# Performance work log

Hardware: AMD Instinct MI355X
Metric: run time of the kernel (lower is better)

## Reference

```python
import jax, jax.numpy as jnp
import numpy as np

BINS = 10
LOSS_WEIGHT = 1.0


def setup_inputs() -> dict:
    key = jax.random.key(0)
    k1, k2 = jax.random.split(key)
    N, C = 32768, 1024
    pred = jax.random.normal(k1, (N, C), dtype=jnp.float32)
    target = jax.random.randint(k2, (N,), 0, C, dtype=jnp.int32)
    return {"pred": pred, "target": target}


def reference(pred, target):
    N, C = pred.shape
    # one-hot target (torch scatter_ of 1 at label index)
    t = jax.nn.one_hot(target, C, dtype=pred.dtype)  # [N, C]
    # gradient norm g = |sigmoid(pred).detach() - target|, in [0, 1]
    g = jnp.abs(jax.nn.sigmoid(jax.lax.stop_gradient(pred)) - t)
    # all samples valid (label_weight=None -> ones); tot = max(sum(valid), 1)
    tot = jnp.asarray(N * C, dtype=pred.dtype)
    # edges = arange(bins+1)/bins with edges[-1] += 1e-6: bin = floor(g*bins),
    # g == 1.0 falls in last bin -> clip to bins-1
    bin_idx = jnp.clip((g * BINS).astype(jnp.int32), 0, BINS - 1)  # [N, C]
    counts = jnp.bincount(bin_idx.ravel(), length=BINS).astype(pred.dtype)  # [BINS]
    nonempty = counts > 0
    n = jnp.maximum(jnp.sum(nonempty).astype(pred.dtype), 1.0)
    # per-bin weight tot/num_in_bin for nonempty bins, then divide by n
    w_bin = jnp.where(nonempty, tot / jnp.maximum(counts, 1.0), 0.0) / n
    weights = w_bin[bin_idx]  # gather back to [N, C]
    # stable BCE-with-logits, weighted, reduction='sum'
    bce = jnp.maximum(pred, 0.0) - pred * t + jnp.log1p(jnp.exp(-jnp.abs(pred)))
    loss = jnp.sum(weights * bce) / tot
    return loss * LOSS_WEIGHT
```

## Files before the change

### kernel.cpp

```cpp
#include <hip/hip_runtime.h>
#include <math.h>


#define PASS1_BLOCK 256

__device__ __forceinline__ void wave_red(float& v) {
#pragma unroll
    for (int off = 32; off > 0; off >>= 1) v += __shfl_down(v, off, 64);
}
__device__ __forceinline__ void wave_red(unsigned& v) {
#pragma unroll
    for (int off = 32; off > 0; off >>= 1) v += __shfl_down(v, off, 64);
}

__device__ __forceinline__ void update_elem(float p, bool isT,
                                            float (&S)[10], unsigned (&Cc)[9]) {
    const float T[9] = {-2.1972246f, -1.3862944f, -0.84729786f, -0.40546511f,
                        0.0f, 0.40546511f, 0.84729786f, 1.3862944f, 2.1972246f};
    float s = isT ? -p : p;
    float a = fabsf(s);
    float en = __expf(-a);
    float bce = fmaxf(s, 0.0f) + __logf(1.0f + en);
    S[0] += bce;
#pragma unroll
    for (int q = 0; q < 9; ++q) {
        bool b = (s >= T[q]);
        S[q + 1] += b ? bce : 0.0f;
        Cc[q] += b ? 1u : 0u;
    }
}

__global__ __launch_bounds__(PASS1_BLOCK) void ghmc_pass1(
    const float* __restrict__ pred, const int* __restrict__ target,
    float* __restrict__ blk_S, unsigned* __restrict__ blk_C,
    unsigned total4, unsigned totalNC, int C, int shift) {
    float S[10];
    unsigned Cc[9];
#pragma unroll
    for (int i = 0; i < 10; ++i) S[i] = 0.0f;
#pragma unroll
    for (int i = 0; i < 9; ++i) Cc[i] = 0u;

    unsigned tid = blockIdx.x * blockDim.x + threadIdx.x;
    unsigned stride = gridDim.x * blockDim.x;
    const float4* p4 = (const float4*)pred;
    unsigned cmask = (unsigned)C - 1u;

    for (unsigned v = tid; v < total4; v += stride) {
        unsigned e = v << 2;
        unsigned row, col;
        if (shift >= 0) {
            row = e >> shift;
            col = e & cmask;
        } else {
            row = e / (unsigned)C;
            col = e - row * (unsigned)C;
        }
        float4 p = p4[v];
        int tj = target[row];
        update_elem(p.x, tj == (int)(col + 0u), S, Cc);
        update_elem(p.y, tj == (int)(col + 1u), S, Cc);
        update_elem(p.z, tj == (int)(col + 2u), S, Cc);
        update_elem(p.w, tj == (int)(col + 3u), S, Cc);
    }

    if (tid == 0) {
        for (unsigned e = total4 << 2; e < totalNC; ++e) {
            unsigned row, col;
            if (shift >= 0) {
                row = e >> shift;
                col = e & cmask;
            } else {
                row = e / (unsigned)C;
                col = e - row * (unsigned)C;
            }
            update_elem(pred[e], target[row] == (int)col, S, Cc);
        }
    }

#pragma unroll
    for (int i = 0; i < 10; ++i) wave_red(S[i]);
#pragma unroll
    for (int i = 0; i < 9; ++i) wave_red(Cc[i]);

    __shared__ float sS[PASS1_BLOCK / 64][10];
    __shared__ unsigned sC[PASS1_BLOCK / 64][9];
    int wid = threadIdx.x >> 6;
    int lane = threadIdx.x & 63;
    if (lane == 0) {
        for (int i = 0; i < 10; ++i) sS[wid][i] = S[i];
        for (int i = 0; i < 9; ++i) sC[wid][i] = Cc[i];
    }
    __syncthreads();
    if (threadIdx.x == 0) {
        const int nw = PASS1_BLOCK / 64;
        for (int i = 0; i < 10; ++i) {
            float acc = 0.0f;
            for (int w = 0; w < nw; ++w) acc += sS[w][i];
            blk_S[blockIdx.x * 10 + i] = acc;
        }
        for (int i = 0; i < 9; ++i) {
            unsigned acc = 0u;
            for (int w = 0; w < nw; ++w) acc += sC[w][i];
            blk_C[blockIdx.x * 9 + i] = acc;
        }
    }
}

__global__ __launch_bounds__(256) void ghmc_pass2(
    const float* __restrict__ blk_S, const unsigned* __restrict__ blk_C,
    float* __restrict__ out, int nblocks, unsigned totalNC) {
    float S[10];
    unsigned Cc[9];
#pragma unroll
    for (int i = 0; i < 10; ++i) S[i] = 0.0f;
#pragma unroll
    for (int i = 0; i < 9; ++i) Cc[i] = 0u;

    for (int b = threadIdx.x; b < nblocks; b += blockDim.x) {
        for (int i = 0; i < 10; ++i) S[i] += blk_S[b * 10 + i];
        for (int i = 0; i < 9; ++i) Cc[i] += blk_C[b * 9 + i];
    }

#pragma unroll
    for (int i = 0; i < 10; ++i) wave_red(S[i]);
#pragma unroll
    for (int i = 0; i < 9; ++i) wave_red(Cc[i]);

    __shared__ float sS[4][10];
    __shared__ unsigned sC[4][9];
    int wid = threadIdx.x >> 6;
    int lane = threadIdx.x & 63;
    if (lane == 0) {
        for (int i = 0; i < 10; ++i) sS[wid][i] = S[i];
        for (int i = 0; i < 9; ++i) sC[wid][i] = Cc[i];
    }
    __syncthreads();
    if (threadIdx.x == 0) {
        float Sv[11];
        unsigned Cv[11];
        for (int i = 0; i < 10; ++i) {
            float a = 0.0f;
            for (int w = 0; w < 4; ++w) a += sS[w][i];
            Sv[i] = a;
        }
        Sv[10] = 0.0f;
        Cv[0] = totalNC;
        for (int i = 1; i < 10; ++i) {
            unsigned a = 0u;
            for (int w = 0; w < 4; ++w) a += sC[w][i - 1];
            Cv[i] = a;
        }
        Cv[10] = 0u;

        int nonempty = 0;
        for (int b = 0; b < 10; ++b)
            if (Cv[b] - Cv[b + 1] > 0u) nonempty++;
        float n = fmaxf((float)nonempty, 1.0f);

        float loss = 0.0f;
        for (int b = 0; b < 10; ++b) {
            unsigned cnt = Cv[b] - Cv[b + 1];
            if (cnt > 0u) {
                float bs = Sv[b] - Sv[b + 1];
                loss += bs / ((float)cnt * n);
            }
        }
        out[0] = loss;
    }
}

extern "C" void kernel_launch(void* const* d_in, const int* in_sizes, int n_in,
                              void* d_out, int out_size, void* d_ws, size_t ws_size,
                              hipStream_t stream) {
    const float* pred = (const float*)d_in[0];
    const int* target = (const int*)d_in[1];
    int NC = in_sizes[0];
    int N = in_sizes[1];
    int C = NC / N;
    unsigned total4 = (unsigned)(NC / 4);
    int shift = ((C & (C - 1)) == 0) ? (__builtin_ctz((unsigned)C) + 0) : -1;

    int blocks = 1024;
    size_t per_block = (10 + 9) * sizeof(float);
    if (ws_size < (size_t)blocks * per_block) {
        size_t maxb = ws_size / per_block;
        blocks = (int)(maxb > 0 ? maxb : 1);
    }

    float* blk_S = (float*)d_ws;
    unsigned* blk_C = (unsigned*)((char*)d_ws + (size_t)blocks * 10 * sizeof(float));

    ghmc_pass1<<<blocks, PASS1_BLOCK, 0, stream>>>(pred, target, blk_S, blk_C,
                                                   total4, (unsigned)NC, C, shift);
    ghmc_pass2<<<1, 256, 0, stream>>>(blk_S, blk_C, (float*)d_out, blocks,
                                      (unsigned)NC);
}
```

Measured before the change: 210.4 us.

## Treat all elements as non-target and apply a per-row target correction

The hot loop no longer computes row and column indices or loads the target per element. Every element is processed as if its one-hot label were 0. A separate per-row step then reads the target logit once and adds the difference between the target and non-target BCE and bin contributions. Bin sums and counts are packed into 2-wide float vectors so the compiler can emit packed FMAs. The change also uses nontemporal vector loads and a doubled grid. Counts become floats, which trades exactness at very large totals for cheaper packed arithmetic. The correction assumes the grid has at least as many threads as there are rows.

New measurement: 218.5 us. +3.9%, slower.

```diff
diff --git a/kernel.cpp b/kernel.cpp
--- a/kernel.cpp
+++ b/kernel.cpp
@@ -3,167 +3,157 @@
 
 
 #define PASS1_BLOCK 256
+#define PASS1_GRID 2048
+
+typedef float v2f __attribute__((ext_vector_type(2)));
+typedef float v4f __attribute__((ext_vector_type(4)));
 
 __device__ __forceinline__ void wave_red(float& v) {
 #pragma unroll
     for (int off = 32; off > 0; off >>= 1) v += __shfl_down(v, off, 64);
 }
-__device__ __forceinline__ void wave_red(unsigned& v) {
-#pragma unroll
-    for (int off = 32; off > 0; off >>= 1) v += __shfl_down(v, off, 64);
-}
 
-__device__ __forceinline__ void update_elem(float p, bool isT,
-                                            float (&S)[10], unsigned (&Cc)[9]) {
-    const float T[9] = {-2.1972246f, -1.3862944f, -0.84729786f, -0.40546511f,
-                        0.0f, 0.40546511f, 0.84729786f, 1.3862944f, 2.1972246f};
-    float s = isT ? -p : p;
-    float a = fabsf(s);
+__device__ __constant__ float kThresh[9] = {
+    -2.1972246f, -1.3862944f, -0.84729786f, -0.40546511f, 0.0f,
+    0.40546511f, 0.84729786f, 1.3862944f, 2.1972246f};
+
+__device__ __forceinline__ void upd(float p, float& S0, v2f (&A)[9]) {
+    float a = fabsf(p);
     float en = __expf(-a);
-    float bce = fmaxf(s, 0.0f) + __logf(1.0f + en);
-    S[0] += bce;
+    float l1p = __logf(1.0f + en);
+    float bce = fmaxf(p, 0.0f) + l1p;
+    S0 += bce;
+    v2f bv = {bce, 1.0f};
 #pragma unroll
     for (int q = 0; q < 9; ++q) {
-        bool b = (s >= T[q]);
-        S[q + 1] += b ? bce : 0.0f;
-        Cc[q] += b ? 1u : 0u;
+        float m = (p >= kThresh[q]) ? 1.0f : 0.0f;
+        v2f mv = {m, m};
+        A[q] += bv * mv;
     }
 }
 
-__global__ __launch_bounds__(PASS1_BLOCK) void ghmc_pass1(
+__device__ __forceinline__ void upd_corr(float p, float& S0, v2f (&A)[9]) {
+    float a = fabsf(p);
+    float en = __expf(-a);
+    float l1p = __logf(1.0f + en);
+    float bf = fmaxf(p, 0.0f) + l1p;
+    float bt = fmaxf(-p, 0.0f) + l1p;
+    S0 += bt - bf;
+#pragma unroll
+    for (int q = 0; q < 9; ++q) {
+        float mf = (p >= kThresh[q]) ? 1.0f : 0.0f;
+        float mt = (-p >= kThresh[q]) ? 1.0f : 0.0f;
+        v2f d = {mt * bt - mf * bf, mt - mf};
+        A[q] += d;
+    }
+}
+
+__global__ __launch_bounds__(PASS1_BLOCK, 8) void ghmc_pass1(
     const float* __restrict__ pred, const int* __restrict__ target,
-    float* __restrict__ blk_S, unsigned* __restrict__ blk_C,
-    unsigned total4, unsigned totalNC, int C, int shift) {
-    float S[10];
-    unsigned Cc[9];
+    float* __restrict__ blk, unsigned total4, unsigned totalNC, int N, int C) {
+    float S0 = 0.0f;
+    v2f A[9];
 #pragma unroll
-    for (int i = 0; i < 10; ++i) S[i] = 0.0f;
-#pragma unroll
-    for (int i = 0; i < 9; ++i) Cc[i] = 0u;
+    for (int i = 0; i < 9; ++i) A[i] = (v2f){0.0f, 0.0f};
 
     unsigned tid = blockIdx.x * blockDim.x + threadIdx.x;
     unsigned stride = gridDim.x * blockDim.x;
-    const float4* p4 = (const float4*)pred;
-    unsigned cmask = (unsigned)C - 1u;
+    const v4f* p4 = (const v4f*)pred;
 
     for (unsigned v = tid; v < total4; v += stride) {
-        unsigned e = v << 2;
-        unsigned row, col;
-        if (shift >= 0) {
-            row = e >> shift;
-            col = e & cmask;
-        } else {
-            row = e / (unsigned)C;
-            col = e - row * (unsigned)C;
-        }
-        float4 p = p4[v];
-        int tj = target[row];
-        update_elem(p.x, tj == (int)(col + 0u), S, Cc);
-        update_elem(p.y, tj == (int)(col + 1u), S, Cc);
-        update_elem(p.z, tj == (int)(col + 2u), S, Cc);
-        update_elem(p.w, tj == (int)(col + 3u), S, Cc);
+        v4f p = __builtin_nontemporal_load(p4 + v);
+        upd(p[0], S0, A);
+        upd(p[1], S0, A);
+        upd(p[2], S0, A);
+        upd(p[3], S0, A);
     }
 
     if (tid == 0) {
-        for (unsigned e = total4 << 2; e < totalNC; ++e) {
-            unsigned row, col;
-            if (shift >= 0) {
-                row = e >> shift;
-                col = e & cmask;
-            } else {
-                row = e / (unsigned)C;
-                col = e - row * (unsigned)C;
-            }
-            update_elem(pred[e], target[row] == (int)col, S, Cc);
-        }
+        for (unsigned e = total4 << 2; e < totalNC; ++e) upd(pred[e], S0, A);
     }
 
+    int row = (int)(blockIdx.x * blockDim.x + threadIdx.x);
+    if (row < N) {
+        int t = target[row];
+        float p = pred[(unsigned)row * (unsigned)C + (unsigned)t];
+        upd_corr(p, S0, A);
+    }
+
+    float vals[19];
+    vals[0] = S0;
 #pragma unroll
-    for (int i = 0; i < 10; ++i) wave_red(S[i]);
+    for (int i = 0; i < 9; ++i) {
+        vals[1 + i] = A[i].x;
+        vals[10 + i] = A[i].y;
+    }
 #pragma unroll
-    for (int i = 0; i < 9; ++i) wave_red(Cc[i]);
+    for (int i = 0; i < 19; ++i) wave_red(vals[i]);
 
-    __shared__ float sS[PASS1_BLOCK / 64][10];
-    __shared__ unsigned sC[PASS1_BLOCK / 64][9];
+    __shared__ float sP[PASS1_BLOCK / 64][19];
     int wid = threadIdx.x >> 6;
     int lane = threadIdx.x & 63;
     if (lane == 0) {
-        for (int i = 0; i < 10; ++i) sS[wid][i] = S[i];
-        for (int i = 0; i < 9; ++i) sC[wid][i] = Cc[i];
+#pragma unroll
+        for (int i = 0; i < 19; ++i) sP[wid][i] = vals[i];
     }
     __syncthreads();
     if (threadIdx.x == 0) {
         const int nw = PASS1_BLOCK / 64;
-        for (int i = 0; i < 10; ++i) {
+#pragma unroll
+        for (int i = 0; i < 19; ++i) {
             float acc = 0.0f;
-            for (int w = 0; w < nw; ++w) acc += sS[w][i];
-            blk_S[blockIdx.x * 10 + i] = acc;
-        }
-        for (int i = 0; i < 9; ++i) {
-            unsigned acc = 0u;
-            for (int w = 0; w < nw; ++w) acc += sC[w][i];
-            blk_C[blockIdx.x * 9 + i] = acc;
+            for (int w = 0; w < nw; ++w) acc += sP[w][i];
+            blk[(unsigned)blockIdx.x * 19u + (unsigned)i] = acc;
         }
     }
 }
 
 __global__ __launch_bounds__(256) void ghmc_pass2(
-    const float* __restrict__ blk_S, const unsigned* __restrict__ blk_C,
-    float* __restrict__ out, int nblocks, unsigned totalNC) {
-    float S[10];
-    unsigned Cc[9];
+    const float* __restrict__ blk, float* __restrict__ out, int nblocks,
+    float totalNC) {
+    float P[19];
 #pragma unroll
-    for (int i = 0; i < 10; ++i) S[i] = 0.0f;
-#pragma unroll
-    for (int i = 0; i < 9; ++i) Cc[i] = 0u;
+    for (int i = 0; i < 19; ++i) P[i] = 0.0f;
 
     for (int b = threadIdx.x; b < nblocks; b += blockDim.x) {
-        for (int i = 0; i < 10; ++i) S[i] += blk_S[b * 10 + i];
-        for (int i = 0; i < 9; ++i) Cc[i] += blk_C[b * 9 + i];
+#pragma unroll
+        for (int i = 0; i < 19; ++i) P[i] += blk[(unsigned)b * 19u + (unsigned)i];
     }
+#pragma unroll
+    for (int i = 0; i < 19; ++i) wave_red(P[i]);
 
-#pragma unroll
-    for (int i = 0; i < 10; ++i) wave_red(S[i]);
-#pragma unroll
-    for (int i = 0; i < 9; ++i) wave_red(Cc[i]);
-
-    __shared__ float sS[4][10];
-    __shared__ unsigned sC[4][9];
+    __shared__ float sP[4][19];
     int wid = threadIdx.x >> 6;
     int lane = threadIdx.x & 63;
     if (lane == 0) {
-        for (int i = 0; i < 10; ++i) sS[wid][i] = S[i];
-        for (int i = 0; i < 9; ++i) sC[wid][i] = Cc[i];
+#pragma unroll
+        for (int i = 0; i < 19; ++i) sP[wid][i] = P[i];
     }
     __syncthreads();
     if (threadIdx.x == 0) {
-        float Sv[11];
-        unsigned Cv[11];
-        for (int i = 0; i < 10; ++i) {
+        float Sv[11], Cv[11];
+        for (int i = 0; i < 19; ++i) {
             float a = 0.0f;
-            for (int w = 0; w < 4; ++w) a += sS[w][i];
-            Sv[i] = a;
+            for (int w = 0; w < 4; ++w) a += sP[w][i];
+            P[i] = a;
         }
+        for (int i = 0; i < 10; ++i) Sv[i] = P[i];
         Sv[10] = 0.0f;
         Cv[0] = totalNC;
-        for (int i = 1; i < 10; ++i) {
-            unsigned a = 0u;
-            for (int w = 0; w < 4; ++w) a += sC[w][i - 1];
-            Cv[i] = a;
-        }
-        Cv[10] = 0u;
+        for (int i = 1; i < 10; ++i) Cv[i] = P[9 + i];
+        Cv[10] = 0.0f;
 
         int nonempty = 0;
         for (int b = 0; b < 10; ++b)
-            if (Cv[b] - Cv[b + 1] > 0u) nonempty++;
+            if (Cv[b] - Cv[b + 1] > 0.5f) nonempty++;
         float n = fmaxf((float)nonempty, 1.0f);
 
         float loss = 0.0f;
         for (int b = 0; b < 10; ++b) {
-            unsigned cnt = Cv[b] - Cv[b + 1];
-            if (cnt > 0u) {
+            float cnt = Cv[b] - Cv[b + 1];
+            if (cnt > 0.5f) {
                 float bs = Sv[b] - Sv[b + 1];
-                loss += bs / ((float)cnt * n);
+                loss += bs / (cnt * n);
             }
         }
         out[0] = loss;
@@ -179,20 +169,17 @@
     int N = in_sizes[1];
     int C = NC / N;
     unsigned total4 = (unsigned)(NC / 4);
-    int shift = ((C & (C - 1)) == 0) ? (__builtin_ctz((unsigned)C) + 0) : -1;
 
-    int blocks = 1024;
-    size_t per_block = (10 + 9) * sizeof(float);
+    int blocks = PASS1_GRID;
+    size_t per_block = 19 * sizeof(float);
     if (ws_size < (size_t)blocks * per_block) {
         size_t maxb = ws_size / per_block;
         blocks = (int)(maxb > 0 ? maxb : 1);
     }
 
-    float* blk_S = (float*)d_ws;
-    unsigned* blk_C = (unsigned*)((char*)d_ws + (size_t)blocks * 10 * sizeof(float));
+    float* blkbuf = (float*)d_ws;
 
-    ghmc_pass1<<<blocks, PASS1_BLOCK, 0, stream>>>(pred, target, blk_S, blk_C,
-                                                   total4, (unsigned)NC, C, shift);
-    ghmc_pass2<<<1, 256, 0, stream>>>(blk_S, blk_C, (float*)d_out, blocks,
-                                      (unsigned)NC);
+    ghmc_pass1<<<blocks, PASS1_BLOCK, 0, stream>>>(pred, target, blkbuf, total4,
+                                                   (unsigned)NC, N, C);
+    ghmc_pass2<<<1, 256, 0, stream>>>(blkbuf, (float*)d_out, blocks, (float)NC);
 }
```
